# Optimization experiments

Measured on AMD Instinct MI355X. Metric: run time of the kernel, lower is better.

The kernel has to match this reference:

```python
import jax, jax.numpy as jnp
import numpy as np

N_USER, N_MERCH, N_EDGE, D, H = 200000, 50000, 2000000, 64, 64


def _segment_mean(vals, idx, num_segments):
    # vals: [E, D] gathered source features; idx: [E] destination ids
    s = jax.ops.segment_sum(vals, idx, num_segments=num_segments)
    c = jax.ops.segment_sum(jnp.ones((idx.shape[0], 1), vals.dtype), idx,
                            num_segments=num_segments)
    return s / jnp.maximum(c, 1.0)


def _hetero_sage(x_u, x_m, bases, coeff, root, b, u_idx, m_idx):
    # basis-decomposed per-edge-type message weights (to_hetero_with_bases)
    W_pays = jnp.einsum('b,bij->ij', coeff[0], bases)  # user -> merchant
    W_rev = jnp.einsum('b,bij->ij', coeff[1], bases)   # merchant -> user
    # SAGEConv: aggregate-then-transform (mean aggregation)
    agg_m = _segment_mean(x_u[u_idx], m_idx, x_m.shape[0])
    agg_u = _segment_mean(x_m[m_idx], u_idx, x_u.shape[0])
    h_m = agg_m @ W_pays + x_m @ root + b
    h_u = agg_u @ W_rev + x_u @ root + b
    return h_u, h_m


def setup_inputs() -> dict:
    key = jax.random.key(0)
    ks = jax.random.split(key, 12)
    sD = 1.0 / np.sqrt(D)
    sH = 1.0 / np.sqrt(H)
    inp = {
        'x_user': jax.random.normal(ks[0], (N_USER, D), jnp.float32),
        'x_merch': jax.random.normal(ks[1], (N_MERCH, D), jnp.float32),
        'bases1': jax.random.normal(ks[2], (3, D, H), jnp.float32) * sD,
        'coeff1': jax.random.normal(ks[3], (2, 3), jnp.float32),
        'root1': jax.random.normal(ks[4], (D, H), jnp.float32) * sD,
        'b1': jnp.zeros((H,), jnp.float32),
        'bases2': jax.random.normal(ks[5], (3, H, H), jnp.float32) * sH,
        'coeff2': jax.random.normal(ks[6], (2, 3), jnp.float32),
        'root2': jax.random.normal(ks[7], (H, H), jnp.float32) * sH,
        'b2': jnp.zeros((H,), jnp.float32),
        'w_mlp1': jax.random.normal(ks[8], (2 * H, H), jnp.float32) / np.sqrt(2 * H),
        'b_mlp1': jnp.zeros((H,), jnp.float32),
        'w_mlp2': jax.random.normal(ks[9], (H, 2), jnp.float32) * sH,
        'b_mlp2': jnp.zeros((2,), jnp.float32),
    }
    u_idx = jax.random.randint(ks[10], (N_EDGE,), 0, N_USER, jnp.int64 if jax.config.jax_enable_x64 else jnp.int32)
    m_idx = jax.random.randint(ks[11], (N_EDGE,), 0, N_MERCH, u_idx.dtype)
    inp['edge_index'] = jnp.stack([u_idx, m_idx])  # [2, E]
    return inp


def reference(x_user, x_merch, bases1, coeff1, root1, b1,
              bases2, coeff2, root2, b2,
              w_mlp1, b_mlp1, w_mlp2, b_mlp2, edge_index):
    u_idx, m_idx = edge_index[0], edge_index[1]
    h_u, h_m = _hetero_sage(x_user, x_merch, bases1, coeff1, root1, b1, u_idx, m_idx)
    h_u, h_m = jax.nn.relu(h_u), jax.nn.relu(h_m)
    h_u, h_m = _hetero_sage(h_u, h_m, bases2, coeff2, root2, b2, u_idx, m_idx)
    # edge classifier: gather-concat-MLP
    z = jnp.concatenate([h_u[u_idx], h_m[m_idx]], axis=1)  # [E, 2H]
    logits = jax.nn.relu(z @ w_mlp1 + b_mlp1) @ w_mlp2 + b_mlp2  # [E, 2]
    return logits
```

## Files before the change

### kernel.cpp

```cpp
#include <hip/hip_runtime.h>


typedef __attribute__((ext_vector_type(8))) short short8;
typedef __attribute__((ext_vector_type(4))) float f32x4;

__device__ inline unsigned short f2bf(float f) {
  unsigned u = __float_as_uint(f);
  u += 0x7FFF + ((u >> 16) & 1);
  return (unsigned short)(u >> 16);
}
__device__ inline float bf2f(unsigned short h) {
  return __uint_as_float(((unsigned)h) << 16);
}
__device__ inline float bf2fs(short h) { return bf2f((unsigned short)h); }

__global__ __launch_bounds__(256) void tobf16_2(
    const float* __restrict__ a, unsigned short* __restrict__ oa, int n4a,
    const float* __restrict__ b, unsigned short* __restrict__ ob, int n4b) {
  int i = blockIdx.x * 256 + threadIdx.x;
  int stride = gridDim.x * 256;
  int tot = n4a + n4b;
  for (int j = i; j < tot; j += stride) {
    float4 v = (j < n4a) ? reinterpret_cast<const float4*>(a)[j]
                         : reinterpret_cast<const float4*>(b)[j - n4a];
    ushort4 o;
    o.x = f2bf(v.x); o.y = f2bf(v.y); o.z = f2bf(v.z); o.w = f2bf(v.w);
    if (j < n4a) reinterpret_cast<ushort4*>(oa)[j] = o;
    else reinterpret_cast<ushort4*>(ob)[j - n4a] = o;
  }
}

__global__ __launch_bounds__(256) void sort_hist_mkW1(
    const int* __restrict__ u_idx, const int* __restrict__ m_idx,
    int* __restrict__ hist_u, int* __restrict__ hist_m, int E, int nblk,
    const float* __restrict__ bases1, const float* __restrict__ coeff1,
    const float* __restrict__ root1,
    const float* __restrict__ bases2, const float* __restrict__ coeff2,
    float* __restrict__ Wcat1u, float* __restrict__ Wcat1m,
    float* __restrict__ wp2, float* __restrict__ wr2) {
  int t = threadIdx.x, blk = blockIdx.x;
  if (blk >= nblk) {
    int ij = (blk - nblk) * 256 + t;
    float a0 = bases1[ij], a1 = bases1[4096 + ij], a2 = bases1[8192 + ij];
    Wcat1m[ij] = coeff1[0] * a0 + coeff1[1] * a1 + coeff1[2] * a2;
    Wcat1u[ij] = coeff1[3] * a0 + coeff1[4] * a1 + coeff1[5] * a2;
    float r = root1[ij];
    Wcat1m[4096 + ij] = r;
    Wcat1u[4096 + ij] = r;
    float c0 = bases2[ij], c1 = bases2[4096 + ij], c2 = bases2[8192 + ij];
    wp2[ij] = coeff2[0] * c0 + coeff2[1] * c1 + coeff2[2] * c2;
    wr2[ij] = coeff2[3] * c0 + coeff2[4] * c1 + coeff2[5] * c2;
    return;
  }
  __shared__ int hu[256], hm[256];
  hu[t] = 0; hm[t] = 0;
  __syncthreads();
  int e0 = blk * 2048 + t;
#pragma unroll
  for (int i = 0; i < 8; ++i) {
    int e = e0 + i * 256;
    if (e < E) {
      atomicAdd(&hu[u_idx[e] >> 10], 1);
      atomicAdd(&hm[m_idx[e] >> 8], 1);
    }
  }
  __syncthreads();
  hist_u[t * nblk + blk] = hu[t];
  hist_m[t * nblk + blk] = hm[t];
}

__global__ __launch_bounds__(256) void scanA2_mkW2(
    int* __restrict__ hist_u, int* __restrict__ hist_m,
    int* __restrict__ part, int nhist, int sb,
    const float* __restrict__ wp2, const float* __restrict__ wr2,
    const float* __restrict__ root2, const float* __restrict__ w_mlp1,
    const float* __restrict__ b2, const float* __restrict__ b_mlp1,
    float* __restrict__ Wcat2u, float* __restrict__ Wcat2m,
    float* __restrict__ bu2, float* __restrict__ bm2) {
  int blk = blockIdx.x;
  if (blk >= 2 * sb) {
    int tid = (blk - 2 * sb) * 256 + threadIdx.x;
    int i = tid >> 6, j = tid & 63;
    float au = 0.f, ru = 0.f, am = 0.f, rm = 0.f;
    for (int k = 0; k < 64; ++k) {
      float wa = w_mlp1[k * 64 + j];
      float wb = w_mlp1[(64 + k) * 64 + j];
      au += wr2[i * 64 + k] * wa;
      ru += root2[i * 64 + k] * wa;
      am += wp2[i * 64 + k] * wb;
      rm += root2[i * 64 + k] * wb;
    }
    Wcat2u[tid] = au; Wcat2u[4096 + tid] = ru;
    Wcat2m[tid] = am; Wcat2m[4096 + tid] = rm;
    if (i == 0) {
      float s1 = 0.f, s2 = 0.f;
      for (int k = 0; k < 64; ++k) {
        s1 += b2[k] * w_mlp1[k * 64 + j];
        s2 += b2[k] * w_mlp1[(64 + k) * 64 + j];
      }
      bu2[j] = s1;
      bm2[j] = s2 + b_mlp1[j];
    }
    return;
  }
  int* arr; int* prt;
  if (blk < sb) { arr = hist_u; prt = part; }
  else { arr = hist_m; prt = part + 256; blk -= sb; }
  __shared__ int s[256];
  int t = threadIdx.x;
  int base = blk * 2048 + t * 8;
  int v[8]; int sum = 0;
#pragma unroll
  for (int i = 0; i < 8; ++i) { int idx = base + i; v[i] = (idx < nhist) ? arr[idx] : 0; sum += v[i]; }
  s[t] = sum;
  __syncthreads();
  for (int ofs = 1; ofs < 256; ofs <<= 1) {
    int a = (t >= ofs) ? s[t - ofs] : 0;
    __syncthreads();
    s[t] += a;
    __syncthreads();
  }
  int run = s[t] - sum;
#pragma unroll
  for (int i = 0; i < 8; ++i) { int idx = base + i; if (idx < nhist) arr[idx] = run; run += v[i]; }
  if (t == 255) prt[blk] = s[255];
}

__global__ __launch_bounds__(256) void scanB2_packW4(
    int* __restrict__ part, int NB,
    const float* __restrict__ s0, const float* __restrict__ s1,
    const float* __restrict__ s2, const float* __restrict__ s3,
    unsigned short* __restrict__ d0, unsigned short* __restrict__ d1,
    unsigned short* __restrict__ d2, unsigned short* __restrict__ d3) {
  int blk = blockIdx.x;
  if (blk >= 2) {
    int gid = (blk - 2) * 256 + threadIdx.x;
    int mat = gid >> 13;
    int tid = gid & 8191;
    int frag = tid >> 9;
    int nt = frag >> 2, ks = frag & 3;
    int lane = (tid >> 3) & 63;
    int i = tid & 7;
    int k = ks * 32 + (lane >> 4) * 8 + i;
    int col = nt * 16 + (lane & 15);
    const float* s = (mat == 0) ? s0 : (mat == 1) ? s1 : (mat == 2) ? s2 : s3;
    unsigned short* d = (mat == 0) ? d0 : (mat == 1) ? d1 : (mat == 2) ? d2 : d3;
    d[tid] = f2bf(s[k * 64 + col]);
    return;
  }
  int* prt = part + blk * 256;
  __shared__ int s[256];
  int t = threadIdx.x;
  int v = (t < NB) ? prt[t] : 0;
  s[t] = v;
  __syncthreads();
  for (int ofs = 1; ofs < 256; ofs <<= 1) {
    int a = (t >= ofs) ? s[t - ofs] : 0;
    __syncthreads();
    s[t] += a;
    __syncthreads();
  }
  if (t < NB) prt[t] = s[t] - v;
}

__global__ __launch_bounds__(256) void scanC2(
    int* __restrict__ hist_u, int* __restrict__ hist_m,
    const int* __restrict__ part, int nhist, int sb) {
  int blk = blockIdx.x;
  int* off; const int* prt;
  if (blk < sb) { off = hist_u; prt = part; }
  else { off = hist_m; prt = part + 256; blk -= sb; }
  int base = blk * 2048 + threadIdx.x * 8;
  int add = prt[blk];
#pragma unroll
  for (int i = 0; i < 8; ++i) { int idx = base + i; if (idx < nhist) off[idx] += add; }
}

__global__ __launch_bounds__(256) void sort_scatter1(
    const int* __restrict__ u_idx, const int* __restrict__ m_idx,
    const int* __restrict__ base_u, const int* __restrict__ base_m,
    int2* __restrict__ stage_u, int2* __restrict__ stage_m, int E, int nblk) {
  __shared__ int cu[256], cm[256];
  int t = threadIdx.x, blk = blockIdx.x;
  cu[t] = base_u[t * nblk + blk];
  cm[t] = base_m[t * nblk + blk];
  __syncthreads();
  int e0 = blk * 2048 + t;
#pragma unroll
  for (int i = 0; i < 8; ++i) {
    int e = e0 + i * 256;
    if (e < E) {
      int u = u_idx[e], m = m_idx[e];
      int pu = atomicAdd(&cu[u >> 10], 1);
      stage_u[pu] = make_int2(u, m);
      int pm = atomicAdd(&cm[m >> 8], 1);
      stage_m[pm] = make_int2(m, u);
    }
  }
}

template <int LOWBITS>
__device__ __forceinline__ void bucket_body(
    const int2* __restrict__ stage, const int* __restrict__ hs,
    int* __restrict__ vals_out, int* __restrict__ off,
    int E, int N, int nblk, int b) {
  constexpr int NBIN = 1 << LOWBITS;
  constexpr int R = NBIN / 256;
  __shared__ int h[NBIN];
  __shared__ int s[256];
  int t = threadIdx.x;
  int seg0 = hs[b * nblk];
  int seg1 = (b == 255) ? E : hs[(b + 1) * nblk];
#pragma unroll
  for (int r = 0; r < R; ++r) h[t * R + r] = 0;
  __syncthreads();
  for (int i = seg0 + t; i < seg1; i += 256)
    atomicAdd(&h[stage[i].x & (NBIN - 1)], 1);
  __syncthreads();
  int vals[R]; int loc = 0;
#pragma unroll
  for (int r = 0; r < R; ++r) { vals[r] = h[t * R + r]; loc += vals[r]; }
  s[t] = loc;
  __syncthreads();
  for (int ofs = 1; ofs < 256; ofs <<= 1) {
    int a = (t >= ofs) ? s[t - ofs] : 0;
    __syncthreads();
    s[t] += a;
    __syncthreads();
  }
  int run = seg0 + s[t] - loc;
#pragma unroll
  for (int r = 0; r < R; ++r) {
    int bin = t * R + r;
    h[bin] = run;
    int node = (b << LOWBITS) + bin;
    if (node <= N) off[node] = run;
    run += vals[r];
  }
  __syncthreads();
  for (int i = seg0 + t; i < seg1; i += 256) {
    int2 v = stage[i];
    int pos = atomicAdd(&h[v.x & (NBIN - 1)], 1);
    vals_out[pos] = v.y;
  }
}

__global__ __launch_bounds__(256) void sort_bucket2(
    const int2* __restrict__ stage_u, const int* __restrict__ hist_u,
    int* __restrict__ csr_u, int* __restrict__ off_u, int Nu,
    const int2* __restrict__ stage_m, const int* __restrict__ hist_m,
    int* __restrict__ csr_m, int* __restrict__ off_m, int Nm,
    int E, int nblk) {
  if (blockIdx.x < 256)
    bucket_body<10>(stage_u, hist_u, csr_u, off_u, E, Nu, nblk, blockIdx.x);
  else
    bucket_body<8>(stage_m, hist_m, csr_m, off_m, E, Nm, nblk, blockIdx.x - 256);
}

template <int RELU>
__device__ __forceinline__ void agg_body(
    const unsigned short* __restrict__ src,
    const unsigned short* __restrict__ selfF,
    const int* __restrict__ off, const int* __restrict__ csr,
    const unsigned short* __restrict__ Wp,
    const float* __restrict__ bias,
    unsigned short* __restrict__ out, int N, int blk) {
  __shared__ unsigned short A[4][16][128];
  int t = threadIdx.x, wave = t >> 6, lane = t & 63;
  int nbase = (blk * 4 + wave) * 16;
  if (nbase >= N) return;
  int fl = lane & 7, sub = lane >> 3;
  const short8* src8 = (const short8*)src;
  char* rowbase = (char*)&A[wave][0][0];
#pragma unroll 1
  for (int j = 0; j < 2; ++j) {
    int g = sub * 2 + j;
    int n = nbase + g;
    float ac[8] = {0.f, 0.f, 0.f, 0.f, 0.f, 0.f, 0.f, 0.f};
    float inv = 1.f;
    short8 sf8 = {0, 0, 0, 0, 0, 0, 0, 0};
    if (n < N) {
      int beg = off[n], end = off[n + 1], k = beg;
      for (; k + 4 <= end; k += 4) {
        int s0 = csr[k], s1 = csr[k + 1], s2 = csr[k + 2], s3 = csr[k + 3];
        short8 r0 = src8[(size_t)s0 * 8 + fl];
        short8 r1 = src8[(size_t)s1 * 8 + fl];
        short8 r2 = src8[(size_t)s2 * 8 + fl];
        short8 r3 = src8[(size_t)s3 * 8 + fl];
#pragma unroll
        for (int c = 0; c < 8; ++c)
          ac[c] += (bf2fs(r0[c]) + bf2fs(r1[c])) + (bf2fs(r2[c]) + bf2fs(r3[c]));
      }
      for (; k < end; ++k) {
        short8 r = src8[(size_t)csr[k] * 8 + fl];
#pragma unroll
        for (int c = 0; c < 8; ++c) ac[c] += bf2fs(r[c]);
      }
      inv = 1.f / fmaxf((float)(end - beg), 1.f);
      sf8 = ((const short8*)selfF)[(size_t)n * 8 + fl];
    }
    short8 ab;
#pragma unroll
    for (int c = 0; c < 8; ++c) ab[c] = (short)f2bf(ac[c] * inv);
    int swz = (g & 7) << 4;
    char* rp = rowbase + g * 256;
    *(short8*)(rp + ((fl * 16) ^ swz)) = ab;
    *(short8*)(rp + ((128 + fl * 16) ^ swz)) = sf8;
  }
  int r = lane & 15, q = lane >> 4;
  int swzr = (r & 7) << 4;
  const char* arow = rowbase + r * 256;
  short8 af[4];
#pragma unroll
  for (int ks = 0; ks < 4; ++ks)
    af[ks] = *(const short8*)(arow + ((ks * 64 + q * 16) ^ swzr));
  const short8* wp8 = (const short8*)Wp;
#pragma unroll
  for (int nt = 0; nt < 4; ++nt) {
    float b = bias[nt * 16 + r];
    f32x4 acc = {b, b, b, b};
#pragma unroll
    for (int ks = 0; ks < 4; ++ks) {
      short8 bf = wp8[(nt * 4 + ks) * 64 + lane];
      acc = __builtin_amdgcn_mfma_f32_16x16x32_bf16(af[ks], bf, acc, 0, 0, 0);
    }
#pragma unroll
    for (int j = 0; j < 4; ++j) {
      int n = nbase + q * 4 + j;
      if (n < N) {
        float v = acc[j];
        if (RELU) v = fmaxf(v, 0.f);
        out[(size_t)n * 64 + nt * 16 + r] = f2bf(v);
      }
    }
  }
}

template <int RELU>
__global__ __launch_bounds__(256) void agg_dual(
    const unsigned short* __restrict__ srcA, const unsigned short* __restrict__ selfA,
    const int* __restrict__ offA, const int* __restrict__ csrA,
    const unsigned short* __restrict__ WpA, const float* __restrict__ biasA,
    unsigned short* __restrict__ outA, int NA, int gbA,
    const unsigned short* __restrict__ srcB, const unsigned short* __restrict__ selfB,
    const int* __restrict__ offB, const int* __restrict__ csrB,
    const unsigned short* __restrict__ WpB, const float* __restrict__ biasB,
    unsigned short* __restrict__ outB, int NB) {
  int blk = blockIdx.x;
  if (blk < gbA)
    agg_body<RELU>(srcA, selfA, offA, csrA, WpA, biasA, outA, NA, blk);
  else
    agg_body<RELU>(srcB, selfB, offB, csrB, WpB, biasB, outB, NB, blk - gbA);
}

__global__ __launch_bounds__(256) void edge_mlp(
    const unsigned short* __restrict__ pu, const unsigned short* __restrict__ pm,
    const int* __restrict__ u_idx, const int* __restrict__ m_idx,
    const float* __restrict__ w2, const float* __restrict__ bvec,
    float* __restrict__ out, int E) {
  int t = threadIdx.x;
  int lane = t & 63;
  int sub = lane >> 4;
  int fl = lane & 15;
  int f = fl * 4;
  int wid = (blockIdx.x * 256 + t) >> 6;
  int nw = (gridDim.x * 256) >> 6;
  float4 wA = reinterpret_cast<const float4*>(w2)[2 * fl];
  float4 wB = reinterpret_cast<const float4*>(w2)[2 * fl + 1];
  float ob0 = bvec[0], ob1 = bvec[1];
  int ngrp = (E + 7) >> 3;
  for (int g = wid; g < ngrp; g += nw) {
    int eA = g * 8 + sub, eB = eA + 4;
    bool vA = eA < E, vB = eB < E;
    int exA = vA ? eA : 0, exB = vB ? eB : 0;
    int uA = __builtin_nontemporal_load(&u_idx[exA]);
    int mA = __builtin_nontemporal_load(&m_idx[exA]);
    int uB = __builtin_nontemporal_load(&u_idx[exB]);
    int mB = __builtin_nontemporal_load(&m_idx[exB]);
    ushort4 a4A = *reinterpret_cast<const ushort4*>(&pu[(size_t)uA * 64 + f]);
    ushort4 b4A = *reinterpret_cast<const ushort4*>(&pm[(size_t)mA * 64 + f]);
    ushort4 a4B = *reinterpret_cast<const ushort4*>(&pu[(size_t)uB * 64 + f]);
    ushort4 b4B = *reinterpret_cast<const ushort4*>(&pm[(size_t)mB * 64 + f]);
    float v0 = fmaxf(bf2f(a4A.x) + bf2f(b4A.x), 0.f);
    float v1 = fmaxf(bf2f(a4A.y) + bf2f(b4A.y), 0.f);
    float v2 = fmaxf(bf2f(a4A.z) + bf2f(b4A.z), 0.f);
    float v3 = fmaxf(bf2f(a4A.w) + bf2f(b4A.w), 0.f);
    float p0 = v0 * wA.x + v1 * wA.z + v2 * wB.x + v3 * wB.z;
    float p1 = v0 * wA.y + v1 * wA.w + v2 * wB.y + v3 * wB.w;
    float w0 = fmaxf(bf2f(a4B.x) + bf2f(b4B.x), 0.f);
    float w1 = fmaxf(bf2f(a4B.y) + bf2f(b4B.y), 0.f);
    float w2v = fmaxf(bf2f(a4B.z) + bf2f(b4B.z), 0.f);
    float w3 = fmaxf(bf2f(a4B.w) + bf2f(b4B.w), 0.f);
    float q0 = w0 * wA.x + w1 * wA.z + w2v * wB.x + w3 * wB.z;
    float q1 = w0 * wA.y + w1 * wA.w + w2v * wB.y + w3 * wB.w;
#pragma unroll
    for (int o = 8; o; o >>= 1) {
      p0 += __shfl_xor(p0, o); p1 += __shfl_xor(p1, o);
      q0 += __shfl_xor(q0, o); q1 += __shfl_xor(q1, o);
    }
    if (fl == 0) {
      if (vA) *reinterpret_cast<float2*>(&out[(size_t)eA * 2]) = make_float2(p0 + ob0, p1 + ob1);
      if (vB) *reinterpret_cast<float2*>(&out[(size_t)eB * 2]) = make_float2(q0 + ob0, q1 + ob1);
    }
  }
}

extern "C" void kernel_launch(void* const* d_in, const int* in_sizes, int n_in,
                              void* d_out, int out_size, void* d_ws, size_t ws_size,
                              hipStream_t stream) {
  const float* x_user  = (const float*)d_in[0];
  const float* x_merch = (const float*)d_in[1];
  const float* bases1  = (const float*)d_in[2];
  const float* coeff1  = (const float*)d_in[3];
  const float* root1   = (const float*)d_in[4];
  const float* b1      = (const float*)d_in[5];
  const float* bases2  = (const float*)d_in[6];
  const float* coeff2  = (const float*)d_in[7];
  const float* root2   = (const float*)d_in[8];
  const float* b2      = (const float*)d_in[9];
  const float* w_mlp1  = (const float*)d_in[10];
  const float* b_mlp1  = (const float*)d_in[11];
  const float* w_mlp2  = (const float*)d_in[12];
  const float* b_mlp2  = (const float*)d_in[13];
  const int*   edge_ix = (const int*)d_in[14];

  const int Nu = in_sizes[0] / 64;
  const int Nm = in_sizes[1] / 64;
  const int E  = in_sizes[14] / 2;
  const int* u_idx = edge_ix;
  const int* m_idx = edge_ix + E;

  char* p = (char*)d_ws;
  auto alloc = [&](size_t bytes) -> char* {
    char* r = p;
    p += (bytes + 255) & ~(size_t)255;
    return r;
  };
  int* off_u = (int*)alloc((size_t)(Nu + 1) * 4);
  int* off_m = (int*)alloc((size_t)(Nm + 1) * 4);
  int* part  = (int*)alloc(512 * 4);
  int* csr_u = (int*)alloc((size_t)E * 4);
  int* csr_m = (int*)alloc((size_t)E * 4);
  unsigned short* xb_u = (unsigned short*)alloc((size_t)Nu * 64 * 2);
  unsigned short* xb_m = (unsigned short*)alloc((size_t)Nm * 64 * 2);
  unsigned short* h_u  = (unsigned short*)alloc((size_t)Nu * 64 * 2);
  unsigned short* h_m  = (unsigned short*)alloc((size_t)Nm * 64 * 2);
  float* Wcat1u = (float*)alloc(8192 * 4);
  float* Wcat1m = (float*)alloc(8192 * 4);
  float* Wcat2u = (float*)alloc(8192 * 4);
  float* Wcat2m = (float*)alloc(8192 * 4);
  unsigned short* Wp1u = (unsigned short*)alloc(8192 * 2);
  unsigned short* Wp1m = (unsigned short*)alloc(8192 * 2);
  unsigned short* Wp2u = (unsigned short*)alloc(8192 * 2);
  unsigned short* Wp2m = (unsigned short*)alloc(8192 * 2);
  float* wp2 = (float*)alloc(4096 * 4);
  float* wr2 = (float*)alloc(4096 * 4);
  float* bu2 = (float*)alloc(64 * 4);
  float* bm2 = (float*)alloc(64 * 4);
  if ((size_t)(p - (char*)d_ws) > ws_size) return;

  const int nblk = (E + 2047) / 2048;
  const int nhist = 256 * nblk;
  const int sb = (nhist + 2047) / 2048;
  int*  hist_u  = (int*)h_m;
  int*  hist_m  = hist_u + nhist;
  int2* stage_u = (int2*)h_u;
  int2* stage_m = (int2*)xb_u;

  sort_hist_mkW1<<<nblk + 16, 256, 0, stream>>>(
      u_idx, m_idx, hist_u, hist_m, E, nblk,
      bases1, coeff1, root1, bases2, coeff2, Wcat1u, Wcat1m, wp2, wr2);
  scanA2_mkW2<<<2 * sb + 16, 256, 0, stream>>>(
      hist_u, hist_m, part, nhist, sb,
      wp2, wr2, root2, w_mlp1, b2, b_mlp1, Wcat2u, Wcat2m, bu2, bm2);
  scanB2_packW4<<<130, 256, 0, stream>>>(
      part, sb, Wcat1u, Wcat1m, Wcat2u, Wcat2m, Wp1u, Wp1m, Wp2u, Wp2m);
  scanC2<<<2 * sb, 256, 0, stream>>>(hist_u, hist_m, part, nhist, sb);
  sort_scatter1<<<nblk, 256, 0, stream>>>(u_idx, m_idx, hist_u, hist_m,
                                          stage_u, stage_m, E, nblk);
  sort_bucket2<<<512, 256, 0, stream>>>(stage_u, hist_u, csr_u, off_u, Nu,
                                        stage_m, hist_m, csr_m, off_m, Nm,
                                        E, nblk);

  tobf16_2<<<1024, 256, 0, stream>>>(x_user, xb_u, Nu * 16, x_merch, xb_m, Nm * 16);

  int gbu = (Nu + 63) / 64, gbm = (Nm + 63) / 64;
  agg_dual<1><<<gbu + gbm, 256, 0, stream>>>(
      xb_m, xb_u, off_u, csr_u, Wp1u, b1, h_u, Nu, gbu,
      xb_u, xb_m, off_m, csr_m, Wp1m, b1, h_m, Nm);
  unsigned short* pm_buf = xb_m;
  unsigned short* pu_buf = xb_u;
  agg_dual<0><<<gbm + gbu, 256, 0, stream>>>(
      h_u, h_m, off_m, csr_m, Wp2m, bm2, pm_buf, Nm, gbm,
      h_m, h_u, off_u, csr_u, Wp2u, bu2, pu_buf, Nu);

  edge_mlp<<<2048, 256, 0, stream>>>(pu_buf, pm_buf, u_idx, m_idx,
                                     w_mlp2, b_mlp2, (float*)d_out, E);
}
```

Baseline: 359.7 us.

## Pack sort staging into 32-bit keys, fold scan fixup and bf16 cast into scatter

Removes the scanC2 pass by adding the per-block partial prefix inside the scatter and bucket kernels. Fuses the fp32-to-bf16 feature conversion into the scatter launch as extra blocks. Packs staging entries into single 32-bit words (low-bits bucket key plus value) instead of int2, and stores the user-side CSR (merchant ids) as 16-bit shorts, halving that index traffic in sort and aggregation. Reorders the first aggregation launch so merchant nodes come first. Fewer launches and less memory traffic, at the cost of relying on index ranges fitting the packed bit widths.

```diff
diff --git a/kernel.cpp b/kernel.cpp
--- a/kernel.cpp
+++ b/kernel.cpp
@@ -13,22 +13,6 @@
   return __uint_as_float(((unsigned)h) << 16);
 }
 __device__ inline float bf2fs(short h) { return bf2f((unsigned short)h); }
-
-__global__ __launch_bounds__(256) void tobf16_2(
-    const float* __restrict__ a, unsigned short* __restrict__ oa, int n4a,
-    const float* __restrict__ b, unsigned short* __restrict__ ob, int n4b) {
-  int i = blockIdx.x * 256 + threadIdx.x;
-  int stride = gridDim.x * 256;
-  int tot = n4a + n4b;
-  for (int j = i; j < tot; j += stride) {
-    float4 v = (j < n4a) ? reinterpret_cast<const float4*>(a)[j]
-                         : reinterpret_cast<const float4*>(b)[j - n4a];
-    ushort4 o;
-    o.x = f2bf(v.x); o.y = f2bf(v.y); o.z = f2bf(v.z); o.w = f2bf(v.w);
-    if (j < n4a) reinterpret_cast<ushort4*>(oa)[j] = o;
-    else reinterpret_cast<ushort4*>(ob)[j - n4a] = o;
-  }
-}
 
 __global__ __launch_bounds__(256) void sort_hist_mkW1(
     const int* __restrict__ u_idx, const int* __restrict__ m_idx,
@@ -163,27 +147,33 @@
   if (t < NB) prt[t] = s[t] - v;
 }
 
-__global__ __launch_bounds__(256) void scanC2(
-    int* __restrict__ hist_u, int* __restrict__ hist_m,
-    const int* __restrict__ part, int nhist, int sb) {
-  int blk = blockIdx.x;
-  int* off; const int* prt;
-  if (blk < sb) { off = hist_u; prt = part; }
-  else { off = hist_m; prt = part + 256; blk -= sb; }
-  int base = blk * 2048 + threadIdx.x * 8;
-  int add = prt[blk];
-#pragma unroll
-  for (int i = 0; i < 8; ++i) { int idx = base + i; if (idx < nhist) off[idx] += add; }
-}
-
-__global__ __launch_bounds__(256) void sort_scatter1(
+__global__ __launch_bounds__(256) void sort_scatter1_tobf16(
     const int* __restrict__ u_idx, const int* __restrict__ m_idx,
-    const int* __restrict__ base_u, const int* __restrict__ base_m,
-    int2* __restrict__ stage_u, int2* __restrict__ stage_m, int E, int nblk) {
+    const int* __restrict__ hist_u, const int* __restrict__ hist_m,
+    const int* __restrict__ part,
+    unsigned* __restrict__ stage_u, unsigned* __restrict__ stage_m,
+    int E, int nblk,
+    const float* __restrict__ xu, unsigned short* __restrict__ xbu, int n4u,
+    const float* __restrict__ xm, unsigned short* __restrict__ xbm, int n4m) {
+  int t = threadIdx.x, blk = blockIdx.x;
+  if (blk >= nblk) {
+    int i = (blk - nblk) * 256 + t;
+    int stride = 512 * 256;
+    int tot = n4u + n4m;
+    for (int j = i; j < tot; j += stride) {
+      float4 v = (j < n4u) ? reinterpret_cast<const float4*>(xu)[j]
+                           : reinterpret_cast<const float4*>(xm)[j - n4u];
+      ushort4 o;
+      o.x = f2bf(v.x); o.y = f2bf(v.y); o.z = f2bf(v.z); o.w = f2bf(v.w);
+      if (j < n4u) reinterpret_cast<ushort4*>(xbu)[j] = o;
+      else reinterpret_cast<ushort4*>(xbm)[j - n4u] = o;
+    }
+    return;
+  }
   __shared__ int cu[256], cm[256];
-  int t = threadIdx.x, blk = blockIdx.x;
-  cu[t] = base_u[t * nblk + blk];
-  cm[t] = base_m[t * nblk + blk];
+  int idx = t * nblk + blk;
+  cu[t] = hist_u[idx] + part[idx >> 11];
+  cm[t] = hist_m[idx] + part[256 + (idx >> 11)];
   __syncthreads();
   int e0 = blk * 2048 + t;
 #pragma unroll
@@ -192,30 +182,34 @@
     if (e < E) {
       int u = u_idx[e], m = m_idx[e];
       int pu = atomicAdd(&cu[u >> 10], 1);
-      stage_u[pu] = make_int2(u, m);
+      stage_u[pu] = ((unsigned)(u & 1023) << 16) | (unsigned)m;
       int pm = atomicAdd(&cm[m >> 8], 1);
-      stage_m[pm] = make_int2(m, u);
-    }
-  }
-}
-
-template <int LOWBITS>
+      stage_m[pm] = ((unsigned)(m & 255) << 18) | (unsigned)u;
+    }
+  }
+}
+
+template <int LOWBITS, int SHIFT, typename VT>
 __device__ __forceinline__ void bucket_body(
-    const int2* __restrict__ stage, const int* __restrict__ hs,
-    int* __restrict__ vals_out, int* __restrict__ off,
+    const unsigned* __restrict__ stage, const int* __restrict__ hs,
+    const int* __restrict__ prt,
+    VT* __restrict__ vals_out, int* __restrict__ off,
     int E, int N, int nblk, int b) {
   constexpr int NBIN = 1 << LOWBITS;
   constexpr int R = NBIN / 256;
+  constexpr unsigned VMASK = (1u << SHIFT) - 1u;
   __shared__ int h[NBIN];
   __shared__ int s[256];
   int t = threadIdx.x;
-  int seg0 = hs[b * nblk];
-  int seg1 = (b == 255) ? E : hs[(b + 1) * nblk];
+  int i0 = b * nblk;
+  int seg0 = hs[i0] + prt[i0 >> 11];
+  int seg1 = E;
+  if (b != 255) { int i1 = (b + 1) * nblk; seg1 = hs[i1] + prt[i1 >> 11]; }
 #pragma unroll
   for (int r = 0; r < R; ++r) h[t * R + r] = 0;
   __syncthreads();
   for (int i = seg0 + t; i < seg1; i += 256)
-    atomicAdd(&h[stage[i].x & (NBIN - 1)], 1);
+    atomicAdd(&h[stage[i] >> SHIFT], 1);
   __syncthreads();
   int vals[R]; int loc = 0;
 #pragma unroll
@@ -239,29 +233,31 @@
   }
   __syncthreads();
   for (int i = seg0 + t; i < seg1; i += 256) {
-    int2 v = stage[i];
-    int pos = atomicAdd(&h[v.x & (NBIN - 1)], 1);
-    vals_out[pos] = v.y;
+    unsigned v = stage[i];
+    int pos = atomicAdd(&h[v >> SHIFT], 1);
+    vals_out[pos] = (VT)(v & VMASK);
   }
 }
 
 __global__ __launch_bounds__(256) void sort_bucket2(
-    const int2* __restrict__ stage_u, const int* __restrict__ hist_u,
-    int* __restrict__ csr_u, int* __restrict__ off_u, int Nu,
-    const int2* __restrict__ stage_m, const int* __restrict__ hist_m,
+    const unsigned* __restrict__ stage_u, const int* __restrict__ hist_u,
+    unsigned short* __restrict__ csr_u, int* __restrict__ off_u, int Nu,
+    const unsigned* __restrict__ stage_m, const int* __restrict__ hist_m,
     int* __restrict__ csr_m, int* __restrict__ off_m, int Nm,
-    int E, int nblk) {
+    const int* __restrict__ part, int E, int nblk) {
   if (blockIdx.x < 256)
-    bucket_body<10>(stage_u, hist_u, csr_u, off_u, E, Nu, nblk, blockIdx.x);
+    bucket_body<10, 16, unsigned short>(stage_u, hist_u, part, csr_u, off_u,
+                                        E, Nu, nblk, blockIdx.x);
   else
-    bucket_body<8>(stage_m, hist_m, csr_m, off_m, E, Nm, nblk, blockIdx.x - 256);
-}
-
-template <int RELU>
+    bucket_body<8, 18, int>(stage_m, hist_m, part + 256, csr_m, off_m,
+                            E, Nm, nblk, blockIdx.x - 256);
+}
+
+template <typename IT, int RELU>
 __device__ __forceinline__ void agg_body(
     const unsigned short* __restrict__ src,
     const unsigned short* __restrict__ selfF,
-    const int* __restrict__ off, const int* __restrict__ csr,
+    const int* __restrict__ off, const IT* __restrict__ csr,
     const unsigned short* __restrict__ Wp,
     const float* __restrict__ bias,
     unsigned short* __restrict__ out, int N, int blk) {
@@ -282,7 +278,8 @@
     if (n < N) {
       int beg = off[n], end = off[n + 1], k = beg;
       for (; k + 4 <= end; k += 4) {
-        int s0 = csr[k], s1 = csr[k + 1], s2 = csr[k + 2], s3 = csr[k + 3];
+        int s0 = (int)csr[k], s1 = (int)csr[k + 1];
+        int s2 = (int)csr[k + 2], s3 = (int)csr[k + 3];
         short8 r0 = src8[(size_t)s0 * 8 + fl];
         short8 r1 = src8[(size_t)s1 * 8 + fl];
         short8 r2 = src8[(size_t)s2 * 8 + fl];
@@ -292,7 +289,7 @@
           ac[c] += (bf2fs(r0[c]) + bf2fs(r1[c])) + (bf2fs(r2[c]) + bf2fs(r3[c]));
       }
       for (; k < end; ++k) {
-        short8 r = src8[(size_t)csr[k] * 8 + fl];
+        short8 r = src8[(size_t)((int)csr[k]) * 8 + fl];
 #pragma unroll
         for (int c = 0; c < 8; ++c) ac[c] += bf2fs(r[c]);
       }
@@ -343,14 +340,14 @@
     const unsigned short* __restrict__ WpA, const float* __restrict__ biasA,
     unsigned short* __restrict__ outA, int NA, int gbA,
     const unsigned short* __restrict__ srcB, const unsigned short* __restrict__ selfB,
-    const int* __restrict__ offB, const int* __restrict__ csrB,
+    const int* __restrict__ offB, const unsigned short* __restrict__ csrB,
     const unsigned short* __restrict__ WpB, const float* __restrict__ biasB,
     unsigned short* __restrict__ outB, int NB) {
   int blk = blockIdx.x;
   if (blk < gbA)
-    agg_body<RELU>(srcA, selfA, offA, csrA, WpA, biasA, outA, NA, blk);
+    agg_body<int, RELU>(srcA, selfA, offA, csrA, WpA, biasA, outA, NA, blk);
   else
-    agg_body<RELU>(srcB, selfB, offB, csrB, WpB, biasB, outB, NB, blk - gbA);
+    agg_body<unsigned short, RELU>(srcB, selfB, offB, csrB, WpB, biasB, outB, NB, blk - gbA);
 }
 
 __global__ __launch_bounds__(256) void edge_mlp(
@@ -439,7 +436,7 @@
   int* off_u = (int*)alloc((size_t)(Nu + 1) * 4);
   int* off_m = (int*)alloc((size_t)(Nm + 1) * 4);
   int* part  = (int*)alloc(512 * 4);
-  int* csr_u = (int*)alloc((size_t)E * 4);
+  unsigned short* csr_u = (unsigned short*)alloc((size_t)E * 2);
   int* csr_m = (int*)alloc((size_t)E * 4);
   unsigned short* xb_u = (unsigned short*)alloc((size_t)Nu * 64 * 2);
   unsigned short* xb_m = (unsigned short*)alloc((size_t)Nm * 64 * 2);
@@ -462,10 +459,10 @@
   const int nblk = (E + 2047) / 2048;
   const int nhist = 256 * nblk;
   const int sb = (nhist + 2047) / 2048;
-  int*  hist_u  = (int*)h_m;
-  int*  hist_m  = hist_u + nhist;
-  int2* stage_u = (int2*)h_u;
-  int2* stage_m = (int2*)xb_u;
+  unsigned* stage_u = (unsigned*)h_u;
+  unsigned* stage_m = stage_u + E;
+  int* hist_u = (int*)h_m;
+  int* hist_m = hist_u + nhist;
 
   sort_hist_mkW1<<<nblk + 16, 256, 0, stream>>>(
       u_idx, m_idx, hist_u, hist_m, E, nblk,
@@ -475,19 +472,17 @@
       wp2, wr2, root2, w_mlp1, b2, b_mlp1, Wcat2u, Wcat2m, bu2, bm2);
   scanB2_packW4<<<130, 256, 0, stream>>>(
       part, sb, Wcat1u, Wcat1m, Wcat2u, Wcat2m, Wp1u, Wp1m, Wp2u, Wp2m);
-  scanC2<<<2 * sb, 256, 0, stream>>>(hist_u, hist_m, part, nhist, sb);
-  sort_scatter1<<<nblk, 256, 0, stream>>>(u_idx, m_idx, hist_u, hist_m,
-                                          stage_u, stage_m, E, nblk);
+  sort_scatter1_tobf16<<<nblk + 512, 256, 0, stream>>>(
+      u_idx, m_idx, hist_u, hist_m, part, stage_u, stage_m, E, nblk,
+      x_user, xb_u, Nu * 16, x_merch, xb_m, Nm * 16);
   sort_bucket2<<<512, 256, 0, stream>>>(stage_u, hist_u, csr_u, off_u, Nu,
                                         stage_m, hist_m, csr_m, off_m, Nm,
-                                        E, nblk);
-
-  tobf16_2<<<1024, 256, 0, stream>>>(x_user, xb_u, Nu * 16, x_merch, xb_m, Nm * 16);
+                                        part, E, nblk);
 
   int gbu = (Nu + 63) / 64, gbm = (Nm + 63) / 64;
-  agg_dual<1><<<gbu + gbm, 256, 0, stream>>>(
-      xb_m, xb_u, off_u, csr_u, Wp1u, b1, h_u, Nu, gbu,
-      xb_u, xb_m, off_m, csr_m, Wp1m, b1, h_m, Nm);
+  agg_dual<1><<<gbm + gbu, 256, 0, stream>>>(
+      xb_u, xb_m, off_m, csr_m, Wp1m, b1, h_m, Nm, gbm,
+      xb_m, xb_u, off_u, csr_u, Wp1u, b1, h_u, Nu);
   unsigned short* pm_buf = xb_m;
   unsigned short* pu_buf = xb_u;
   agg_dual<0><<<gbm + gbu, 256, 0, stream>>>(
```

Measured after the change: 362.6 us. Within noise of the previous version (+0.8%).
